# Optimization experiments

Measured on AMD Instinct MI355X. Metric: run time of the kernel, lower is better.

The kernel has to match this reference:

```python
import jax, jax.numpy as jnp
import numpy as np

N_NODES = 50000
N_EDGES = 600000
IN_F, HID_F, OUT_F = 128, 128, 64


def setup_inputs() -> dict:
    key = jax.random.key(0)
    ks = jax.random.split(key, 7)
    features = jax.random.normal(ks[0], (N_NODES, IN_F), jnp.float32)
    W1 = jax.random.normal(ks[1], (IN_F, HID_F), jnp.float32) / np.sqrt(IN_F)
    b1 = jnp.zeros((HID_F,), jnp.float32)
    W2 = jax.random.normal(ks[2], (HID_F, OUT_F), jnp.float32) / np.sqrt(HID_F)
    b2 = jnp.zeros((OUT_F,), jnp.float32)
    edge_src = jax.random.randint(ks[3], (N_EDGES,), 0, N_NODES, jnp.int32)
    edge_dst = jax.random.randint(ks[4], (N_EDGES,), 0, N_NODES, jnp.int32)
    return {"features": features, "W1": W1, "b1": b1, "W2": W2, "b2": b2,
            "edge_src": edge_src, "edge_dst": edge_dst}


def _graph_conv(h, W, b, edge_src, edge_dst, norm_src, norm_dst, n_nodes):
    # DGL GraphConv, norm='both': D_in^{-1/2} A D_out^{-1/2} (h W) + b
    # Apply W first (linear commutes with the linear aggregation) to minimize
    # the size of the gathered edge tensor when out <= in.
    h = (h * norm_src[:, None]) @ W                       # [N, d_out]
    agg = jax.ops.segment_sum(h[edge_src], edge_dst, num_segments=n_nodes)
    return agg * norm_dst[:, None] + b


def reference(features, W1, b1, W2, b2, edge_src, edge_dst):
    n_nodes = features.shape[0]
    ones = jnp.ones(edge_src.shape[0], features.dtype)
    out_deg = jax.ops.segment_sum(ones, edge_src, num_segments=n_nodes)
    in_deg = jax.ops.segment_sum(ones, edge_dst, num_segments=n_nodes)
    norm_src = jnp.clip(out_deg, 1.0) ** -0.5             # source-side D_out^{-1/2}
    norm_dst = jnp.clip(in_deg, 1.0) ** -0.5              # dest-side   D_in^{-1/2}
    h = _graph_conv(features, W1, b1, edge_src, edge_dst, norm_src, norm_dst, n_nodes)
    h = jax.nn.relu(h)
    h = _graph_conv(h, W2, b2, edge_src, edge_dst, norm_src, norm_dst, n_nodes)
    return h
```

## Files before the change

kernel.cpp:

```cpp
#include <hip/hip_runtime.h>


typedef unsigned short u16;
typedef unsigned int u32;
typedef short s16x8 __attribute__((ext_vector_type(8)));
typedef float f32x4 __attribute__((ext_vector_type(4)));
typedef u32 u32x4 __attribute__((ext_vector_type(4)));

__device__ __forceinline__ float bf2f(u16 u) {
    return __uint_as_float((u32)u << 16);
}
__device__ __forceinline__ u16 f2bf(float f) {
    u32 u = __float_as_uint(f);
    u += 0x7fff + ((u >> 16) & 1);
    return (u16)(u >> 16);
}


__global__ __launch_bounds__(256) void hist_part(const int* __restrict__ src,
                                                 const int* __restrict__ dst,
                                                 u32* __restrict__ part) {
    __shared__ u32 cnt[6250];
    const int s = blockIdx.x;
    const int r = blockIdx.y;
    const int z = blockIdx.z;
    const int lo = r * 12500;
    for (int t = threadIdx.x; t < 6250; t += 256) cnt[t] = 0;
    __syncthreads();
    const int* ids = z ? dst : src;
    const int base = s * 37500;
    for (int e0 = base; e0 < base + 37500; e0 += 1024) {
        int idx[4];
#pragma unroll
        for (int k = 0; k < 4; ++k) {
            int e = e0 + k * 256 + threadIdx.x;
            idx[k] = (e < base + 37500) ? ids[e] : -1;
        }
#pragma unroll
        for (int k = 0; k < 4; ++k) {
            unsigned local = (unsigned)(idx[k] - lo);
            if (local < 12500u)
                atomicAdd(&cnt[local >> 1], 1u << ((local & 1) * 16));
        }
    }
    __syncthreads();
    u32* out = part + (size_t)(z * 16 + s) * 25000 + r * 6250;
    for (int t = threadIdx.x; t < 6250; t += 256) out[t] = cnt[t];
}

__global__ __launch_bounds__(256) void reduce_norm_sniff(const u32* __restrict__ part,
                                                         int* __restrict__ degd,
                                                         float* __restrict__ ns,
                                                         float* __restrict__ nd,
                                                         int* __restrict__ bsum,
                                                         const u16* __restrict__ X16,
                                                         int* __restrict__ flag) {
    __shared__ int sh[256];
    if (blockIdx.x == 0) {
        u16 v = X16[threadIdx.x * 2];
        int e = (v >> 7) & 0xFF;
        sh[threadIdx.x] = (e >= 0x30 && e <= 0x47) ? 1 : 0;
        __syncthreads();
        for (int off = 128; off > 0; off >>= 1) {
            if (threadIdx.x < off) sh[threadIdx.x] += sh[threadIdx.x + off];
            __syncthreads();
        }
        if (threadIdx.x == 0) *flag = (sh[0] >= 128) ? 1 : 0;
        __syncthreads();
    }
    int i = blockIdx.x * 256 + threadIdx.x;
    u32 a = 0, b = 0;
    if (i < 50000) {
        const int w = i >> 1, h = (i & 1) * 16;
#pragma unroll
        for (int s = 0; s < 16; ++s) {
            a += (part[(size_t)s * 25000 + w] >> h) & 0xffffu;
            b += (part[(size_t)(16 + s) * 25000 + w] >> h) & 0xffffu;
        }
        degd[i] = (int)b;
        ns[i] = rsqrtf((float)(a > 1 ? a : 1));
        nd[i] = rsqrtf((float)(b > 1 ? b : 1));
    }
    sh[threadIdx.x] = (i < 50000) ? (int)b : 0;
    __syncthreads();
    for (int off = 128; off > 0; off >>= 1) {
        if (threadIdx.x < off) sh[threadIdx.x] += sh[threadIdx.x + off];
        __syncthreads();
    }
    if (threadIdx.x == 0) bsum[blockIdx.x] = sh[0];
}

__global__ __launch_bounds__(256) void rowptr_scan(const int* __restrict__ degd,
                                                   const int* __restrict__ bsum,
                                                   int* __restrict__ rp,
                                                   int* __restrict__ cur,
                                                   int n, int nb) {
    __shared__ int sb[256];
    __shared__ int sh[256];
    const int t = threadIdx.x;
    sb[t] = (t < nb && t < (int)blockIdx.x) ? bsum[t] : 0;
    int i = blockIdx.x * 256 + t;
    int v = (i < n) ? degd[i] : 0;
    sh[t] = v;
    __syncthreads();
    for (int off = 128; off > 0; off >>= 1) {
        if (t < off) sb[t] += sb[t + off];
        __syncthreads();
    }
    const int boff = sb[0];
    for (int off = 1; off < 256; off <<= 1) {
        int x = (t >= off) ? sh[t - off] : 0;
        __syncthreads();
        sh[t] += x;
        __syncthreads();
    }
    if (i < n) {
        int e = boff + sh[t] - v;
        rp[i] = e;
        cur[i] = e;
        if (i == n - 1) rp[n] = e + v;
    }
}

__global__ __launch_bounds__(256) void fill_kernel(const int* __restrict__ src,
                                                   const int* __restrict__ dst,
                                                   int* __restrict__ cur,
                                                   int* __restrict__ col, int n) {
    int i = blockIdx.x * 256 + threadIdx.x;
    if (i < n) {
        int pos = atomicAdd(&cur[dst[i]], 1);
        col[pos] = src[i];
    }
}

template <int FO, bool X_ALWAYS_BF16>
__global__ __launch_bounds__(256) void gemm_mfma(const void* __restrict__ Xv,
                                                 const void* __restrict__ Wv,
                                                 const int* __restrict__ flagp,
                                                 const float* __restrict__ ns,
                                                 u16* __restrict__ Ylo,
                                                 u16* __restrict__ Yhi,
                                                 int split, int nrows) {
    __shared__ __align__(16) u32 Xs[64 * 68];
    __shared__ __align__(16) u32 Bs[FO * 68];
    const int flag = *flagp;
    const int tid = threadIdx.x;
    const int nb = blockIdx.x * 64;

    const bool xbf = X_ALWAYS_BF16 ? true : (flag != 0);
    if (xbf) {
        const u32* Xg = (const u32*)Xv;
        for (int t = tid; t < 64 * 64; t += 256) {
            int row = t >> 6, cp = t & 63;
            int r = nb + row;
            Xs[row * 68 + cp] = (r < nrows) ? Xg[(size_t)r * 64 + cp] : 0u;
        }
    } else {
        const float* Xg = (const float*)Xv;
        for (int t = tid; t < 64 * 64; t += 256) {
            int row = t >> 6, cp = t & 63;
            int r = nb + row;
            u32 lo = 0, hi = 0;
            if (r < nrows) {
                lo = f2bf(Xg[(size_t)r * 128 + 2 * cp]);
                hi = f2bf(Xg[(size_t)r * 128 + 2 * cp + 1]);
            }
            Xs[row * 68 + cp] = lo | (hi << 16);
        }
    }
    if (flag) {
        const u32* Wg = (const u32*)Wv;
        for (int t = tid; t < FO * 64; t += 256) {
            int col = t >> 6, kp = t & 63;
            u32 lo = Wg[(size_t)(2 * kp) * (FO / 2) + (col >> 1)];
            u32 hi = Wg[(size_t)(2 * kp + 1) * (FO / 2) + (col >> 1)];
            int sh = (col & 1) * 16;
            Bs[col * 68 + kp] = ((lo >> sh) & 0xffffu) | (((hi >> sh) & 0xffffu) << 16);
        }
    } else {
        const float* Wg = (const float*)Wv;
        for (int t = tid; t < FO * 64; t += 256) {
            int col = t >> 6, kp = t & 63;
            u32 lo = f2bf(Wg[(size_t)(2 * kp) * FO + col]);
            u32 hi = f2bf(Wg[(size_t)(2 * kp + 1) * FO + col]);
            Bs[col * 68 + kp] = lo | (hi << 16);
        }
    }
    __syncthreads();

    const int lane = tid & 63;
    const int wv = tid >> 6;
    const int rt = wv * 16;
    const int lr = lane & 15;
    const int g = lane >> 4;

    union U4 { u32x4 u; s16x8 s; };

    U4 a[4];
#pragma unroll
    for (int t = 0; t < 4; ++t)
        a[t].u = *(const u32x4*)&Xs[(rt + lr) * 68 + t * 16 + g * 4];

    const int rq = nb + rt + g * 4;
    float nsv[4];
#pragma unroll
    for (int q = 0; q < 4; ++q) nsv[q] = ns[rq + q];

#pragma unroll
    for (int ct = 0; ct < FO / 16; ++ct) {
        f32x4 acc = {0.f, 0.f, 0.f, 0.f};
#pragma unroll
        for (int t = 0; t < 4; ++t) {
            U4 b;
            b.u = *(const u32x4*)&Bs[(ct * 16 + lr) * 68 + t * 16 + g * 4];
            acc = __builtin_amdgcn_mfma_f32_16x16x32_bf16(a[t].s, b.s, acc,
                                                          0, 0, 0);
        }
        const int cc = ct * 16 + lr;
#pragma unroll
        for (int q = 0; q < 4; ++q) {
            int r = rq + q;
            if (r < nrows) {
                u16* Y = (r < split) ? (Ylo + (size_t)r * FO)
                                     : (Yhi + (size_t)(r - split) * FO);
                Y[cc] = f2bf(acc[q] * nsv[q]);
            }
        }
    }
}

__global__ __launch_bounds__(256) void gather128(const u16* __restrict__ Hlo,
                                                 const u16* __restrict__ Hhi, int split,
                                                 const int* __restrict__ rp,
                                                 const int* __restrict__ col,
                                                 const float* __restrict__ nd,
                                                 const void* __restrict__ bias,
                                                 const int* __restrict__ flagp,
                                                 u16* __restrict__ out, int nnodes) {
    int wv = threadIdx.x >> 6, lane = threadIdx.x & 63;
    int n = blockIdx.x * 4 + wv;
    if (n >= nnodes) return;
    int p0 = rp[n], p1 = rp[n + 1];
    float a0 = 0.f, a1 = 0.f;
    int e = p0;
    for (; e + 8 <= p1; e += 8) {
        u32 u[8];
#pragma unroll
        for (int t = 0; t < 8; ++t) {
            int s = col[e + t];
            const u32* r = (const u32*)((s < split) ? (Hlo + (size_t)s * 128)
                                                    : (Hhi + (size_t)(s - split) * 128));
            u[t] = r[lane];
        }
#pragma unroll
        for (int t = 0; t < 8; ++t) {
            a0 += bf2f((u16)(u[t] & 0xffff));
            a1 += bf2f((u16)(u[t] >> 16));
        }
    }
    for (; e + 4 <= p1; e += 4) {
        u32 u[4];
#pragma unroll
        for (int t = 0; t < 4; ++t) {
            int s = col[e + t];
            const u32* r = (const u32*)((s < split) ? (Hlo + (size_t)s * 128)
                                                    : (Hhi + (size_t)(s - split) * 128));
            u[t] = r[lane];
        }
#pragma unroll
        for (int t = 0; t < 4; ++t) {
            a0 += bf2f((u16)(u[t] & 0xffff));
            a1 += bf2f((u16)(u[t] >> 16));
        }
    }
    for (; e < p1; ++e) {
        int s = col[e];
        const u16* H = (s < split) ? (Hlo + (size_t)s * 128)
                                   : (Hhi + (size_t)(s - split) * 128);
        u32 u = ((const u32*)H)[lane];
        a0 += bf2f((u16)(u & 0xffff));
        a1 += bf2f((u16)(u >> 16));
    }
    int flag = *flagp;
    float bb0 = flag ? bf2f(((const u16*)bias)[lane * 2]) : ((const float*)bias)[lane * 2];
    float bb1 = flag ? bf2f(((const u16*)bias)[lane * 2 + 1]) : ((const float*)bias)[lane * 2 + 1];
    float v = nd[n];
    float o0 = fmaxf(a0 * v + bb0, 0.f);
    float o1 = fmaxf(a1 * v + bb1, 0.f);
    ((u32*)(out + (size_t)n * 128))[lane] = (u32)f2bf(o0) | ((u32)f2bf(o1) << 16);
}

__global__ __launch_bounds__(256) void gather64(const u16* __restrict__ H,
                                                const int* __restrict__ rp,
                                                const int* __restrict__ col,
                                                const float* __restrict__ nd,
                                                const void* __restrict__ bias,
                                                const int* __restrict__ flagp,
                                                void* __restrict__ outv, int nnodes) {
    int wv = threadIdx.x >> 6, lane = threadIdx.x & 63;
    int n = blockIdx.x * 4 + wv;
    if (n >= nnodes) return;
    int p0 = rp[n], p1 = rp[n + 1];
    float a = 0.f;
    int e = p0;
    for (; e + 8 <= p1; e += 8) {
        float f[8];
#pragma unroll
        for (int t = 0; t < 8; ++t)
            f[t] = bf2f(H[(size_t)col[e + t] * 64 + lane]);
#pragma unroll
        for (int t = 0; t < 8; ++t) a += f[t];
    }
    for (; e + 4 <= p1; e += 4) {
        float f[4];
#pragma unroll
        for (int t = 0; t < 4; ++t)
            f[t] = bf2f(H[(size_t)col[e + t] * 64 + lane]);
#pragma unroll
        for (int t = 0; t < 4; ++t) a += f[t];
    }
    for (; e < p1; ++e)
        a += bf2f(H[(size_t)col[e] * 64 + lane]);
    int flag = *flagp;
    float bb = flag ? bf2f(((const u16*)bias)[lane]) : ((const float*)bias)[lane];
    float o = a * nd[n] + bb;
    if (flag)
        ((u16*)outv)[(size_t)n * 64 + lane] = f2bf(o);
    else
        ((float*)outv)[(size_t)n * 64 + lane] = o;
}

extern "C" void kernel_launch(void* const* d_in, const int* in_sizes, int n_in,
                              void* d_out, int out_size, void* d_ws, size_t ws_size,
                              hipStream_t stream) {
    constexpr int N = 50000;
    constexpr int E = 600000;
    constexpr int NB = (N + 255) / 256;
    constexpr int SPLIT = 25000;

    const void* X  = d_in[0];
    const void* W1 = d_in[1];
    const void* b1 = d_in[2];
    const void* W2 = d_in[3];
    const void* b2 = d_in[4];
    const int* esrc = (const int*)d_in[5];
    const int* edst = (const int*)d_in[6];

    char* p = (char*)d_ws;
    auto take = [&](size_t bytes) -> char* {
        char* r = p;
        p += (bytes + 255) & ~(size_t)255;
        return r;
    };
    int* flagp  = (int*)take(256);
    int* deg_d  = (int*)take((size_t)N * 4);
    float* ns   = (float*)take((size_t)N * 4);
    float* nd   = (float*)take((size_t)N * 4);
    int* bsum   = (int*)take((size_t)NB * 4);
    int* rp     = (int*)take((size_t)(N + 1) * 4);
    int* cur    = (int*)take((size_t)N * 4);
    int* col    = (int*)take((size_t)E * 4);
    u16* h0hi   = (u16*)take((size_t)(N - SPLIT) * 128 * 2);
    u16* a2     = (u16*)take((size_t)N * 128 * 2);
    size_t NEED = (size_t)(p - (char*)d_ws);

    if (ws_size < NEED) {
        hipMemsetAsync(d_out, 0, (size_t)out_size * 2, stream);
        return;
    }

    u16* h0lo = (u16*)d_out;

    u32* part = (u32*)a2;

    hist_part<<<dim3(16, 4, 2), 256, 0, stream>>>(esrc, edst, part);
    reduce_norm_sniff<<<NB, 256, 0, stream>>>(part, deg_d, ns, nd, bsum,
                                              (const u16*)X, flagp);
    rowptr_scan<<<NB, 256, 0, stream>>>(deg_d, bsum, rp, cur, N, NB);
    fill_kernel<<<(E + 255) / 256, 256, 0, stream>>>(esrc, edst, cur, col, E);

    gemm_mfma<128, false><<<(N + 63) / 64, 256, 0, stream>>>(
        X, W1, flagp, ns, h0lo, h0hi, SPLIT, N);
    gather128<<<(N + 3) / 4, 256, 0, stream>>>(h0lo, h0hi, SPLIT, rp, col, nd,
                                               b1, flagp, a2, N);

    u16* h1b = h0hi;
    gemm_mfma<64, true><<<(N + 63) / 64, 256, 0, stream>>>(
        a2, W2, flagp, ns, h1b, h1b, N, N);
    gather64<<<(N + 3) / 4, 256, 0, stream>>>(h1b, rp, col, nd, b2, flagp,
                                              d_out, N);

    (void)in_sizes; (void)n_in; (void)out_size;
}
```

Before: 265.6 us.

## Keep W fragments in registers and split GEMM work across waves by columns

The MFMA GEMM no longer stages the weight matrix in shared memory. Each wave now owns a slice of output columns and loads its B fragments straight from global memory into registers. It then loops over all four 16-row tiles, reading X from LDS. This removes the Bs LDS buffer and its repeated LDS reads, but adds many scalar, uncoalesced global loads of W per block and more register pressure.

```diff
diff --git a/kernel.cpp b/kernel.cpp
--- a/kernel.cpp
+++ b/kernel.cpp
@@ -141,8 +141,8 @@
                                                  u16* __restrict__ Ylo,
                                                  u16* __restrict__ Yhi,
                                                  int split, int nrows) {
+    constexpr int NCT = FO / 64;
     __shared__ __align__(16) u32 Xs[64 * 68];
-    __shared__ __align__(16) u32 Bs[FO * 68];
     const int flag = *flagp;
     const int tid = threadIdx.x;
     const int nb = blockIdx.x * 64;
@@ -168,62 +168,78 @@
             Xs[row * 68 + cp] = lo | (hi << 16);
         }
     }
+
+    const int lane = tid & 63;
+    const int wv = tid >> 6;
+    const int lr = lane & 15;
+    const int g = lane >> 4;
+    const int cbase = wv * (FO / 4);
+
+    u32 bf[NCT][4][4];
     if (flag) {
         const u32* Wg = (const u32*)Wv;
-        for (int t = tid; t < FO * 64; t += 256) {
-            int col = t >> 6, kp = t & 63;
-            u32 lo = Wg[(size_t)(2 * kp) * (FO / 2) + (col >> 1)];
-            u32 hi = Wg[(size_t)(2 * kp + 1) * (FO / 2) + (col >> 1)];
-            int sh = (col & 1) * 16;
-            Bs[col * 68 + kp] = ((lo >> sh) & 0xffffu) | (((hi >> sh) & 0xffffu) << 16);
+#pragma unroll
+        for (int c = 0; c < NCT; ++c) {
+            const int col = cbase + c * 16 + lr;
+            const int ce = col >> 1, sh = (col & 1) * 16;
+#pragma unroll
+            for (int t = 0; t < 4; ++t)
+#pragma unroll
+                for (int p = 0; p < 4; ++p) {
+                    const int kp = t * 16 + g * 4 + p;
+                    u32 lo = (Wg[(size_t)(2 * kp) * (FO / 2) + ce] >> sh) & 0xffffu;
+                    u32 hi = (Wg[(size_t)(2 * kp + 1) * (FO / 2) + ce] >> sh) & 0xffffu;
+                    bf[c][t][p] = lo | (hi << 16);
+                }
         }
     } else {
         const float* Wg = (const float*)Wv;
-        for (int t = tid; t < FO * 64; t += 256) {
-            int col = t >> 6, kp = t & 63;
-            u32 lo = f2bf(Wg[(size_t)(2 * kp) * FO + col]);
-            u32 hi = f2bf(Wg[(size_t)(2 * kp + 1) * FO + col]);
-            Bs[col * 68 + kp] = lo | (hi << 16);
+#pragma unroll
+        for (int c = 0; c < NCT; ++c) {
+            const int col = cbase + c * 16 + lr;
+#pragma unroll
+            for (int t = 0; t < 4; ++t)
+#pragma unroll
+                for (int p = 0; p < 4; ++p) {
+                    const int kp = t * 16 + g * 4 + p;
+                    u32 lo = f2bf(Wg[(size_t)(2 * kp) * FO + col]);
+                    u32 hi = f2bf(Wg[(size_t)(2 * kp + 1) * FO + col]);
+                    bf[c][t][p] = lo | (hi << 16);
+                }
         }
     }
     __syncthreads();
 
-    const int lane = tid & 63;
-    const int wv = tid >> 6;
-    const int rt = wv * 16;
-    const int lr = lane & 15;
-    const int g = lane >> 4;
-
     union U4 { u32x4 u; s16x8 s; };
-
-    U4 a[4];
-#pragma unroll
-    for (int t = 0; t < 4; ++t)
-        a[t].u = *(const u32x4*)&Xs[(rt + lr) * 68 + t * 16 + g * 4];
-
-    const int rq = nb + rt + g * 4;
-    float nsv[4];
-#pragma unroll
-    for (int q = 0; q < 4; ++q) nsv[q] = ns[rq + q];
-
-#pragma unroll
-    for (int ct = 0; ct < FO / 16; ++ct) {
-        f32x4 acc = {0.f, 0.f, 0.f, 0.f};
-#pragma unroll
-        for (int t = 0; t < 4; ++t) {
-            U4 b;
-            b.u = *(const u32x4*)&Bs[(ct * 16 + lr) * 68 + t * 16 + g * 4];
-            acc = __builtin_amdgcn_mfma_f32_16x16x32_bf16(a[t].s, b.s, acc,
-                                                          0, 0, 0);
-        }
-        const int cc = ct * 16 + lr;
-#pragma unroll
-        for (int q = 0; q < 4; ++q) {
-            int r = rq + q;
-            if (r < nrows) {
-                u16* Y = (r < split) ? (Ylo + (size_t)r * FO)
-                                     : (Yhi + (size_t)(r - split) * FO);
-                Y[cc] = f2bf(acc[q] * nsv[q]);
+#pragma unroll
+    for (int rt = 0; rt < 4; ++rt) {
+        U4 a[4];
+#pragma unroll
+        for (int t = 0; t < 4; ++t)
+            a[t].u = *(const u32x4*)&Xs[(rt * 16 + lr) * 68 + t * 16 + g * 4];
+        const int rq = nb + rt * 16 + g * 4;
+        float nsv[4];
+#pragma unroll
+        for (int q = 0; q < 4; ++q) nsv[q] = ns[rq + q];
+#pragma unroll
+        for (int c = 0; c < NCT; ++c) {
+            f32x4 acc = {0.f, 0.f, 0.f, 0.f};
+#pragma unroll
+            for (int t = 0; t < 4; ++t) {
+                U4 b;
+                b.u = (u32x4){bf[c][t][0], bf[c][t][1], bf[c][t][2], bf[c][t][3]};
+                acc = __builtin_amdgcn_mfma_f32_16x16x32_bf16(a[t].s, b.s, acc,
+                                                              0, 0, 0);
+            }
+            const int cc = cbase + c * 16 + lr;
+#pragma unroll
+            for (int q = 0; q < 4; ++q) {
+                int r = rq + q;
+                if (r < nrows) {
+                    u16* Y = (r < split) ? (Ylo + (size_t)r * FO)
+                                         : (Yhi + (size_t)(r - split) * FO);
+                    Y[cc] = f2bf(acc[q] * nsv[q]);
+                }
             }
         }
     }
```

New measurement: 225.8 us. -15.0%, faster.
